# Kernel optimization log

Hardware: AMD Instinct MI355X
Metric: run time of the kernel (lower is better)

The kernel has to match this reference:

```python
import jax, jax.numpy as jnp
import numpy as np

LN_EPS = 1e-12


def _layernorm(x, gamma, beta):
    mu = jnp.mean(x, axis=-1, keepdims=True)
    var = jnp.mean((x - mu) ** 2, axis=-1, keepdims=True)
    return (x - mu) * jax.lax.rsqrt(var + LN_EPS) * gamma + beta


def _gcn(x, node_emb, time_emb, wpool, bpool, ln_g, ln_b):
    # x: [B,N,C]; node_emb: [N,D]; time_emb: [D]
    e = _layernorm(node_emb + time_emb[None, :], ln_g, ln_b)          # [N,D] (dropout in eval = identity)
    adj = jax.nn.softmax(e @ e.T, axis=1)                             # [N,N] dynamic adjacency
    weights = jnp.einsum('nd,dkio->nkio', e, wpool)                   # [N,2,Cin,Cout] per-node weights
    bias = e @ bpool                                                  # [N,Cout]
    # supports = [I, adj]: identity support is just x itself
    x_g = jnp.stack([x, jnp.einsum('nm,bmc->bnc', adj, x)], axis=2)   # [B,N,2,Cin]
    return jnp.einsum('bnki,nkio->bno', x_g, weights) + bias          # [B,N,Cout]


def setup_inputs() -> dict:
    key = jax.random.key(0)
    ks = jax.random.split(key, 10)
    B, N, Cin, H, D = 32, 2048, 32, 64, 64
    s = 0.1
    return {
        'x': jax.random.normal(ks[0], (B, N, Cin), jnp.float32),
        'state': jax.random.normal(ks[1], (B, N, H), jnp.float32),
        'node_embeddings': jax.random.normal(ks[2], (N, D), jnp.float32),
        'time_embeddings': jax.random.normal(ks[3], (D,), jnp.float32),
        'gate_wpool': jax.random.normal(ks[4], (D, 2, Cin + H, 2 * H), jnp.float32) * s,
        'gate_bpool': jax.random.normal(ks[5], (D, 2 * H), jnp.float32) * s,
        'gate_ln_g': jnp.ones((D,), jnp.float32),
        'gate_ln_b': jnp.zeros((D,), jnp.float32),
        'update_wpool': jax.random.normal(ks[6], (D, 2, Cin + H, H), jnp.float32) * s,
        'update_bpool': jax.random.normal(ks[7], (D, H), jnp.float32) * s,
        'update_ln_g': jnp.ones((D,), jnp.float32),
        'update_ln_b': jnp.zeros((D,), jnp.float32),
    }


def reference(x, state, node_embeddings, time_embeddings,
              gate_wpool, gate_bpool, gate_ln_g, gate_ln_b,
              update_wpool, update_bpool, update_ln_g, update_ln_b):
    H = state.shape[-1]
    inp = jnp.concatenate([x, state], axis=-1)                        # [B,N,Cin+H]
    z_r = jax.nn.sigmoid(_gcn(inp, node_embeddings, time_embeddings,
                              gate_wpool, gate_bpool, gate_ln_g, gate_ln_b))
    z, r = z_r[..., :H], z_r[..., H:]
    cand = jnp.concatenate([x, z * state], axis=-1)
    hc = jnp.tanh(_gcn(cand, node_embeddings, time_embeddings,
                       update_wpool, update_bpool, update_ln_g, update_ln_b))
    return r * state + (1.0 - r) * hc
```

## Files before the change

### kernel.cpp

```cpp
#include <hip/hip_runtime.h>

typedef _Float16 f16;
typedef _Float16 half8 __attribute__((ext_vector_type(8)));
typedef float f32x4 __attribute__((ext_vector_type(4)));

#define NN 2048
#define BB 32
#define CINC 32
#define HH 64
#define DD 64
#define C1 96
#define KI 192
#define OG 128
#define OU 64
#define WCG 24576
#define WCU 12288

#define XGI(n, ks, b, kk) (((((size_t)(n)) * 6 + (ks)) * BB + (b)) * 32 + (kk))

__device__ __forceinline__ f32x4 mfma16(half8 a, half8 b, f32x4 c) {
  return __builtin_amdgcn_mfma_f32_16x16x32_f16(a, b, c, 0, 0, 0);
}

typedef __attribute__((address_space(1))) const void* gas_t;
typedef __attribute__((address_space(3))) void* las_t;
__device__ __forceinline__ void gl_lds16(const void* g, void* l) {
  __builtin_amdgcn_global_load_lds((gas_t)g, (las_t)l, 16, 0, 0);
}

#define SWZ(row, kb) (((row) << 7) + ((kb) ^ (((row) & 7) << 4)))

__global__ __launch_bounds__(256) void k_ln_bias(
    const float* __restrict__ ne, const float* __restrict__ te,
    const float* __restrict__ gg, const float* __restrict__ gb,
    const float* __restrict__ ug, const float* __restrict__ ub,
    const float* __restrict__ gbp, const float* __restrict__ ubp,
    float* __restrict__ eg, float* __restrict__ eu,
    f16* __restrict__ egh, f16* __restrict__ euh,
    float* __restrict__ biasg, float* __restrict__ biasu) {
  __shared__ float esg[4][64];
  __shared__ float esu[4][64];
  int nl = threadIdx.x >> 6;
  int node = blockIdx.x * 4 + nl;
  int d = threadIdx.x & 63;
  float v = ne[node * DD + d] + te[d];
  float s = v;
  #pragma unroll
  for (int m = 1; m < 64; m <<= 1) s += __shfl_xor(s, m, 64);
  float mu = s * (1.f / 64.f);
  float df = v - mu;
  float q = df * df;
  #pragma unroll
  for (int m = 1; m < 64; m <<= 1) q += __shfl_xor(q, m, 64);
  float rs = rsqrtf(q * (1.f / 64.f) + 1e-12f);
  float base = df * rs;
  float a = base * gg[d] + gb[d];
  float b = base * ug[d] + ub[d];
  eg[node * DD + d] = a; egh[node * DD + d] = (f16)a;
  eu[node * DD + d] = b; euh[node * DD + d] = (f16)b;
  esg[nl][d] = a; esu[nl][d] = b;
  __syncthreads();
  #pragma unroll
  for (int i = 0; i < 3; ++i) {
    int u = i * 256 + threadIdx.x;
    int un = u / 192, oo = u % 192;
    int n2 = blockIdx.x * 4 + un;
    float acc = 0.f;
    if (oo < OG) {
      #pragma unroll 8
      for (int dd = 0; dd < 64; ++dd) acc += esg[un][dd] * gbp[dd * OG + oo];
      biasg[(size_t)n2 * OG + oo] = acc;
    } else {
      int o = oo - OG;
      #pragma unroll 8
      for (int dd = 0; dd < 64; ++dd) acc += esu[un][dd] * ubp[dd * OU + o];
      biasu[(size_t)n2 * OU + o] = acc;
    }
  }
}

__global__ __launch_bounds__(256) void k_wpool_t(const float* __restrict__ gwp,
                                                 const float* __restrict__ uwp,
                                                 f16* __restrict__ wtg,
                                                 f16* __restrict__ wtu) {
  const int upd = blockIdx.z;
  if (upd && blockIdx.y >= OU / 16) return;
  const float* wpool = upd ? uwp : gwp;
  f16* wt = upd ? wtu : wtg;
  const int O = upd ? OU : OG;
  __shared__ float tile[64][17];
  int ki = blockIdx.x;
  int o0 = blockIdx.y * 16;
  int t = threadIdx.x;
  const int ks = ki >> 5, kk = ki & 31;
  #pragma unroll
  for (int i = 0; i < 4; ++i) {
    int e2 = i * 256 + t;
    int d = e2 >> 4, o = e2 & 15;
    tile[d][o] = wpool[((size_t)d * KI + ki) * O + o0 + o];
  }
  __syncthreads();
  #pragma unroll
  for (int i = 0; i < 4; ++i) {
    int e2 = i * 256 + t;
    int o = e2 >> 6, d = e2 & 63;
    size_t row = ((size_t)ks * O + (o0 + o)) * 32 + kk;
    wt[row * DD + d] = (f16)tile[d][o];
  }
}

__global__ __launch_bounds__(256) void k_build_inp(const float* __restrict__ x,
                                                   const float* __restrict__ st,
                                                   f16* __restrict__ cm,
                                                   f16* __restrict__ xg,
                                                   f16* __restrict__ sth) {
  __shared__ f16 tile[96][66];
  int mb = blockIdx.x * 64;
  int b = blockIdx.y;
  int t = threadIdx.x;
  #pragma unroll
  for (int i = 0; i < 24; ++i) {
    int e2 = i * 256 + t;
    int m = e2 / 96, c = e2 % 96;
    float v = (c < CINC) ? x[((size_t)b * NN + mb + m) * CINC + c]
                         : st[((size_t)b * NN + mb + m) * HH + c - CINC];
    f16 h = (f16)v;
    tile[c][m] = h;
    xg[XGI(mb + m, c >> 5, b, c & 31)] = h;
    if (c >= CINC) sth[((size_t)b * NN + mb + m) * HH + c - CINC] = h;
  }
  __syncthreads();
  #pragma unroll
  for (int i = 0; i < 24; ++i) {
    int e2 = i * 256 + t;
    int c = e2 >> 6, m = e2 & 63;
    cm[((size_t)b * C1 + c) * NN + mb + m] = tile[c][m];
  }
}

__global__ __launch_bounds__(256) void k_transpose_zs(const f16* __restrict__ zs,
                                                      f16* __restrict__ cm) {
  __shared__ f16 tile[64][66];
  int mb = blockIdx.x * 64;
  int b = blockIdx.y;
  int t = threadIdx.x;
  #pragma unroll
  for (int i = 0; i < 16; ++i) {
    int e2 = i * 256 + t;
    int m = e2 >> 6, o = e2 & 63;
    tile[o][m] = zs[((size_t)b * NN + mb + m) * HH + o];
  }
  __syncthreads();
  #pragma unroll
  for (int i = 0; i < 16; ++i) {
    int e2 = i * 256 + t;
    int o = e2 >> 6, m = e2 & 63;
    cm[((size_t)b * C1 + CINC + o) * NN + mb + m] = tile[o][m];
  }
}

__global__ __launch_bounds__(256) void k_scores(const float* __restrict__ e,
                                                float* __restrict__ S) {
  __shared__ float er[32][65];
  __shared__ float ec[32][65];
  int rb = blockIdx.y * 32, cbb = blockIdx.x * 32;
  int t = threadIdx.x;
  {
    int row = t >> 3;
    int d0 = (t & 7) * 8;
    const float* pr = &e[(size_t)(rb + row) * DD + d0];
    const float* pc = &e[(size_t)(cbb + row) * DD + d0];
    #pragma unroll
    for (int j = 0; j < 8; ++j) { er[row][d0 + j] = pr[j]; ec[row][d0 + j] = pc[j]; }
  }
  __syncthreads();
  int r = t >> 5;
  int c = t & 31;
  float a0 = 0.f, a1 = 0.f, a2 = 0.f, a3 = 0.f;
  #pragma unroll 8
  for (int d = 0; d < 64; ++d) {
    float vc = ec[c][d];
    a0 += er[r][d] * vc;
    a1 += er[r + 8][d] * vc;
    a2 += er[r + 16][d] * vc;
    a3 += er[r + 24][d] * vc;
  }
  S[(size_t)(rb + r) * NN + cbb + c] = a0;
  S[(size_t)(rb + r + 8) * NN + cbb + c] = a1;
  S[(size_t)(rb + r + 16) * NN + cbb + c] = a2;
  S[(size_t)(rb + r + 24) * NN + cbb + c] = a3;
}

__global__ __launch_bounds__(256) void k_softmax(const float* __restrict__ S,
                                                 f16* __restrict__ adj) {
  int n = blockIdx.x;
  int t = threadIdx.x;
  const float* row = S + (size_t)n * NN;
  float v[8];
  float mx = -3.0e38f;
  #pragma unroll
  for (int i = 0; i < 8; ++i) { v[i] = row[t + i * 256]; mx = fmaxf(mx, v[i]); }
  #pragma unroll
  for (int m = 1; m < 64; m <<= 1) mx = fmaxf(mx, __shfl_xor(mx, m, 64));
  __shared__ float redm[4];
  if ((t & 63) == 0) redm[t >> 6] = mx;
  __syncthreads();
  mx = fmaxf(fmaxf(redm[0], redm[1]), fmaxf(redm[2], redm[3]));
  float s = 0.f;
  #pragma unroll
  for (int i = 0; i < 8; ++i) { v[i] = expf(v[i] - mx); s += v[i]; }
  #pragma unroll
  for (int m = 1; m < 64; m <<= 1) s += __shfl_xor(s, m, 64);
  __shared__ float reds[4];
  if ((t & 63) == 0) reds[t >> 6] = s;
  __syncthreads();
  s = reds[0] + reds[1] + reds[2] + reds[3];
  float inv = 1.f / s;
  #pragma unroll
  for (int i = 0; i < 8; ++i) adj[(size_t)n * NN + t + i * 256] = (f16)(v[i] * inv);
}

#define BM 64
#define BN 96

__global__ __launch_bounds__(256, 4) void k_gemm_xa(const f16* __restrict__ A,
                                                    const f16* __restrict__ Bm,
                                                    f16* __restrict__ xg) {
  const int orig = blockIdx.x;
  const int xcd = orig & 7, j = orig >> 3;
  const int nb = (j >> 2) * BM;
  const int by = (xcd << 2) + (j & 3);
  const int cb = by * BN;
  const int tid = threadIdx.x;
  const int w = tid >> 6, lane = tid & 63;
  const int wr = (w >> 1) * 32, wc = (w & 1) * 48;
  const int fr = lane & 15, fq = lane >> 4;

  const int arow = tid >> 3;
  const int acolb = ((tid & 7) * 16) ^ ((arow & 7) << 4);
  const char* asrc = (const char*)A + (size_t)(nb + arow) * (NN * 2) + acolb;
  const char* bsrc = (const char*)Bm + (size_t)(cb + arow) * (NN * 2) + acolb;

  __shared__ f16 Al[2][BM * 64];
  __shared__ f16 Bl[2][BN * 64];
  auto stage = [&](int buf, int kt) {
    const size_t ko = (size_t)kt * 2;
    char* ad = (char*)&Al[buf][0] + (w << 10);
    char* bd = (char*)&Bl[buf][0] + (w << 10);
    gl_lds16(asrc + ko, ad);
    gl_lds16(asrc + ko + (size_t)32 * (NN * 2), ad + 4096);
    gl_lds16(bsrc + ko, bd);
    gl_lds16(bsrc + ko + (size_t)32 * (NN * 2), bd + 4096);
    gl_lds16(bsrc + ko + (size_t)64 * (NN * 2), bd + 8192);
  };

  f32x4 acc[2][3] = {};
  stage(0, 0);
  for (int kt = 0; kt < NN; kt += 64) {
    const int cur = (kt >> 6) & 1;
    if (kt + 64 < NN) {
      stage(cur ^ 1, kt + 64);
      asm volatile("s_waitcnt vmcnt(5)" ::: "memory");
    } else {
      asm volatile("s_waitcnt vmcnt(0)" ::: "memory");
    }
    __builtin_amdgcn_sched_barrier(0);
    __builtin_amdgcn_s_barrier();
    const char* Ab = (const char*)&Al[cur][0];
    const char* Bb = (const char*)&Bl[cur][0];
    half8 af[2][2], bf[2][3];
    #pragma unroll
    for (int k0 = 0; k0 < 2; ++k0) {
      const int kb = k0 * 64 + fq * 16;
      #pragma unroll
      for (int mt = 0; mt < 2; ++mt)
        af[k0][mt] = *(const half8*)(Ab + SWZ(wr + mt * 16 + fr, kb));
      #pragma unroll
      for (int nt = 0; nt < 3; ++nt)
        bf[k0][nt] = *(const half8*)(Bb + SWZ(wc + nt * 16 + fr, kb));
    }
    asm volatile("s_waitcnt lgkmcnt(0)" ::: "memory");
    __builtin_amdgcn_sched_barrier(0);
    __builtin_amdgcn_s_barrier();
    #pragma unroll
    for (int k0 = 0; k0 < 2; ++k0)
      #pragma unroll
      for (int mt = 0; mt < 2; ++mt)
        #pragma unroll
        for (int nt = 0; nt < 3; ++nt)
          acc[mt][nt] = mfma16(af[k0][mt], bf[k0][nt], acc[mt][nt]);
  }
  #pragma unroll
  for (int mt = 0; mt < 2; ++mt)
    #pragma unroll
    for (int nt = 0; nt < 3; ++nt)
      #pragma unroll
      for (int r = 0; r < 4; ++r) {
        int n = nb + wr + mt * 16 + fq * 4 + r;
        int l = wc + nt * 16 + fr;
        xg[XGI(n, 3 + (l >> 5), by, l & 31)] = (f16)acc[mt][nt][r];
      }
}

__global__ __launch_bounds__(256) void k_gemm_w2(const f16* __restrict__ A,
                                                 const f16* __restrict__ B,
                                                 f16* __restrict__ W, int ncols) {
  __shared__ f16 Al[128 * 64];
  __shared__ f16 Bl[128 * 64];
  const int cb = blockIdx.x * 128;
  const int nb = blockIdx.y * 128;
  const int tid = threadIdx.x;
  const int w = tid >> 6, lane = tid & 63;
  const int wr = (w >> 1) * 64, wc = (w & 1) * 64;
  const int fr = lane & 15, fq = lane >> 4;
  const int arow = tid >> 3;
  const int acolb = ((tid & 7) * 16) ^ ((arow & 7) << 4);
  const char* asrc = (const char*)A + (size_t)(nb + arow) * 128 + acolb;
  const char* bsrc = (const char*)B + (size_t)(cb + arow) * 128 + acolb;
  char* ad = (char*)Al + (w << 10);
  char* bd = (char*)Bl + (w << 10);
  #pragma unroll
  for (int j = 0; j < 4; ++j) gl_lds16(asrc + (size_t)j * 32 * 128, ad + j * 4096);
  #pragma unroll
  for (int j = 0; j < 4; ++j) gl_lds16(bsrc + (size_t)j * 32 * 128, bd + j * 4096);
  __syncthreads();
  f32x4 acc[4][4] = {};
  #pragma unroll
  for (int k0 = 0; k0 < 2; ++k0) {
    const int kb = k0 * 64 + fq * 16;
    half8 af[4], bf[4];
    #pragma unroll
    for (int mt = 0; mt < 4; ++mt)
      af[mt] = *(const half8*)((const char*)Al + SWZ(wr + mt * 16 + fr, kb));
    #pragma unroll
    for (int nt = 0; nt < 4; ++nt)
      bf[nt] = *(const half8*)((const char*)Bl + SWZ(wc + nt * 16 + fr, kb));
    #pragma unroll
    for (int mt = 0; mt < 4; ++mt)
      #pragma unroll
      for (int nt = 0; nt < 4; ++nt)
        acc[mt][nt] = mfma16(af[mt], bf[nt], acc[mt][nt]);
  }
  #pragma unroll
  for (int mt = 0; mt < 4; ++mt)
    #pragma unroll
    for (int nt = 0; nt < 4; ++nt)
      #pragma unroll
      for (int r = 0; r < 4; ++r) {
        int n = nb + wr + mt * 16 + fq * 4 + r;
        int c = cb + wc + nt * 16 + fr;
        W[(size_t)n * ncols + c] = (f16)acc[mt][nt][r];
      }
}

template <bool GATE>
__global__ __launch_bounds__(256) void k_apply3(
    const f16* __restrict__ xg, const f16* __restrict__ W,
    const float* __restrict__ bias,
    const f16* __restrict__ sth,
    f16* xgw, f16* __restrict__ zs, f16* __restrict__ rbuf,
    float* __restrict__ outp) {
  constexpr int O = GATE ? OG : OU;
  constexpr int WS = GATE ? WCG : WCU;
  constexpr int NOT_ = GATE ? 2 : 1;
  const int n = blockIdx.x;
  const int lane = threadIdx.x & 63, w = threadIdx.x >> 6;
  const int fr = lane & 15, fq = lane >> 4;
  half8 af[2][6];
  #pragma unroll
  for (int mt = 0; mt < 2; ++mt) {
    #pragma unroll
    for (int ks = 0; ks < 6; ++ks)
      af[mt][ks] = *(const half8*)&xg[XGI(n, ks, mt * 16 + fr, fq * 8)];
  }
  if (GATE) __syncthreads();
  f32x4 acc[2][NOT_] = {};
  #pragma unroll
  for (int ks = 0; ks < 6; ++ks) {
    #pragma unroll
    for (int ot = 0; ot < NOT_; ++ot) {
      int o = (GATE ? (w * 2 + ot) : w) * 16 + fr;
      half8 bf = *(const half8*)&W[(size_t)n * WS + (((size_t)ks * O + o) << 5) + fq * 8];
      #pragma unroll
      for (int mt = 0; mt < 2; ++mt) acc[mt][ot] = mfma16(af[mt][ks], bf, acc[mt][ot]);
    }
  }
  #pragma unroll
  for (int mt = 0; mt < 2; ++mt)
    #pragma unroll
    for (int ot = 0; ot < NOT_; ++ot) {
      const int o = (GATE ? (w * 2 + ot) : w) * 16 + fr;
      const float bs = bias[(size_t)n * O + o];
      #pragma unroll
      for (int r = 0; r < 4; ++r) {
        int b = mt * 16 + fq * 4 + r;
        float val = acc[mt][ot][r] + bs;
        if (GATE) {
          float s = 1.f / (1.f + expf(-val));
          if (o < HH) {
            size_t bno = ((size_t)b * NN + n) * HH + o;
            float zst = s * (float)sth[bno];
            xgw[XGI(n, 1 + (o >> 5), b, o & 31)] = (f16)zst;
            zs[bno] = (f16)zst;
          } else {
            rbuf[((size_t)b * NN + n) * HH + (o - HH)] = (f16)s;
          }
        } else {
          size_t bno = ((size_t)b * NN + n) * HH + o;
          float hc = tanhf(val);
          float rr = (float)rbuf[bno];
          outp[bno] = rr * (float)sth[bno] + (1.f - rr) * hc;
        }
      }
    }
}

extern "C" void kernel_launch(void* const* d_in, const int* in_sizes, int n_in,
                              void* d_out, int out_size, void* d_ws, size_t ws_size,
                              hipStream_t stream) {
  const float* x   = (const float*)d_in[0];
  const float* st  = (const float*)d_in[1];
  const float* ne  = (const float*)d_in[2];
  const float* te  = (const float*)d_in[3];
  const float* gwp = (const float*)d_in[4];
  const float* gbp = (const float*)d_in[5];
  const float* gg  = (const float*)d_in[6];
  const float* gb  = (const float*)d_in[7];
  const float* uwp = (const float*)d_in[8];
  const float* ubp = (const float*)d_in[9];
  const float* ug  = (const float*)d_in[10];
  const float* ub  = (const float*)d_in[11];
  float* out = (float*)d_out;

  char* wsb = (char*)d_ws;
  size_t off = 0;
  auto alloc = [&](size_t bytes) {
    char* p = wsb + off;
    off = (off + bytes + 255) & ~(size_t)255;
    return p;
  };
  float* e_g   = (float*)alloc((size_t)NN * DD * 4);
  float* e_u   = (float*)alloc((size_t)NN * DD * 4);
  f16*   egh   = (f16*)  alloc((size_t)NN * DD * 2);
  f16*   euh   = (f16*)  alloc((size_t)NN * DD * 2);
  float* biasg = (float*)alloc((size_t)NN * OG * 4);
  float* biasu = (float*)alloc((size_t)NN * OU * 4);
  f16*   wtg   = (f16*)  alloc((size_t)WCG * DD * 2);
  f16*   wtu   = (f16*)  alloc((size_t)WCU * DD * 2);
  f16*   xg    = (f16*)  alloc((size_t)NN * BB * KI * 2);
  f16*   cm    = (f16*)  alloc((size_t)BB * C1 * NN * 2);
  f16*   zs    = (f16*)  alloc((size_t)BB * NN * HH * 2);
  f16*   rbuf  = (f16*)  alloc((size_t)BB * NN * HH * 2);
  f16*   sth   = (f16*)  alloc((size_t)BB * NN * HH * 2);
  f16*   adj   = (f16*)  alloc((size_t)NN * NN * 2);
  char*  Wreg  =         alloc((size_t)NN * WCG * 2);
  float* S     = (float*)Wreg;
  f16*   W     = (f16*)Wreg;
  (void)ws_size; (void)in_sizes; (void)n_in; (void)out_size;

  hipLaunchKernelGGL(k_ln_bias, dim3(NN / 4), dim3(256), 0, stream,
                     ne, te, gg, gb, ug, ub, gbp, ubp,
                     e_g, e_u, egh, euh, biasg, biasu);
  hipLaunchKernelGGL(k_wpool_t, dim3(KI, OG / 16, 2), dim3(256), 0, stream,
                     gwp, uwp, wtg, wtu);
  hipLaunchKernelGGL(k_build_inp, dim3(NN / 64, BB), dim3(256), 0, stream,
                     x, st, cm, xg, sth);

  hipLaunchKernelGGL(k_scores, dim3(NN / 32, NN / 32), dim3(256), 0, stream, e_g, S);
  hipLaunchKernelGGL(k_softmax, dim3(NN), dim3(256), 0, stream, S, adj);
  hipLaunchKernelGGL(k_gemm_xa, dim3(1024), dim3(256), 0, stream, adj, cm, xg);
  hipLaunchKernelGGL(k_gemm_w2, dim3(WCG / 128, NN / 128), dim3(256), 0, stream,
                     egh, wtg, W, WCG);
  hipLaunchKernelGGL((k_apply3<true>), dim3(NN), dim3(256), 0, stream,
                     xg, W, biasg, sth, xg, zs, rbuf, (float*)nullptr);
  hipLaunchKernelGGL(k_transpose_zs, dim3(NN / 64, BB), dim3(256), 0, stream, zs, cm);

  hipLaunchKernelGGL(k_scores, dim3(NN / 32, NN / 32), dim3(256), 0, stream, e_u, S);
  hipLaunchKernelGGL(k_softmax, dim3(NN), dim3(256), 0, stream, S, adj);
  hipLaunchKernelGGL(k_gemm_xa, dim3(1024), dim3(256), 0, stream, adj, cm, xg);
  hipLaunchKernelGGL(k_gemm_w2, dim3(WCU / 128, NN / 128), dim3(256), 0, stream,
                     euh, wtu, W, WCU);
  hipLaunchKernelGGL((k_apply3<false>), dim3(NN), dim3(256), 0, stream,
                     xg, W, biasu, sth, (f16*)nullptr, (f16*)nullptr, rbuf, out);
}
```

Before: 234.7 us.

## Fuse per-node weight generation into apply kernel, dropping materialized W buffer

Replaces the separate GEMM that materializes per-node weights W (NN x 24576 fp16, ~100MB for gate) plus the apply kernel with a fused kernel. It computes 16 nodes' weight slices into LDS via MFMA and immediately applies them to the batch inputs. Each block handles one 32-wide output quarter for 16 nodes, with blocks mapped by XCD index to share the weight pool. This removes the large global write and read of W. The cost is recomputing weights per output quarter, extra LDS traffic, and two-blocks-per-CU occupancy limits. The z*state write into xg moves into the transpose kernel, and S gets its own buffer.

```diff
diff --git a/kernel.cpp b/kernel.cpp
--- a/kernel.cpp
+++ b/kernel.cpp
@@ -2,6 +2,7 @@
 
 typedef _Float16 f16;
 typedef _Float16 half8 __attribute__((ext_vector_type(8)));
+typedef _Float16 half4 __attribute__((ext_vector_type(4)));
 typedef float f32x4 __attribute__((ext_vector_type(4)));
 
 #define NN 2048
@@ -13,8 +14,6 @@
 #define KI 192
 #define OG 128
 #define OU 64
-#define WCG 24576
-#define WCU 12288
 
 #define XGI(n, ks, b, kk) (((((size_t)(n)) * 6 + (ks)) * BB + (b)) * 32 + (kk))
 
@@ -92,7 +91,6 @@
   int ki = blockIdx.x;
   int o0 = blockIdx.y * 16;
   int t = threadIdx.x;
-  const int ks = ki >> 5, kk = ki & 31;
   #pragma unroll
   for (int i = 0; i < 4; ++i) {
     int e2 = i * 256 + t;
@@ -104,8 +102,7 @@
   for (int i = 0; i < 4; ++i) {
     int e2 = i * 256 + t;
     int o = e2 >> 6, d = e2 & 63;
-    size_t row = ((size_t)ks * O + (o0 + o)) * 32 + kk;
-    wt[row * DD + d] = (f16)tile[d][o];
+    wt[((size_t)(o0 + o) * KI + ki) * DD + d] = (f16)tile[d][o];
   }
 }
 
@@ -139,7 +136,8 @@
 }
 
 __global__ __launch_bounds__(256) void k_transpose_zs(const f16* __restrict__ zs,
-                                                      f16* __restrict__ cm) {
+                                                      f16* __restrict__ cm,
+                                                      f16* __restrict__ xg) {
   __shared__ f16 tile[64][66];
   int mb = blockIdx.x * 64;
   int b = blockIdx.y;
@@ -148,7 +146,9 @@
   for (int i = 0; i < 16; ++i) {
     int e2 = i * 256 + t;
     int m = e2 >> 6, o = e2 & 63;
-    tile[o][m] = zs[((size_t)b * NN + mb + m) * HH + o];
+    f16 v = zs[((size_t)b * NN + mb + m) * HH + o];
+    tile[o][m] = v;
+    xg[XGI(mb + m, 1 + (o >> 5), b, o & 31)] = v;
   }
   __syncthreads();
   #pragma unroll
@@ -302,117 +302,105 @@
       }
 }
 
-__global__ __launch_bounds__(256) void k_gemm_w2(const f16* __restrict__ A,
-                                                 const f16* __restrict__ B,
-                                                 f16* __restrict__ W, int ncols) {
-  __shared__ f16 Al[128 * 64];
-  __shared__ f16 Bl[128 * 64];
-  const int cb = blockIdx.x * 128;
-  const int nb = blockIdx.y * 128;
-  const int tid = threadIdx.x;
-  const int w = tid >> 6, lane = tid & 63;
-  const int wr = (w >> 1) * 64, wc = (w & 1) * 64;
-  const int fr = lane & 15, fq = lane >> 4;
-  const int arow = tid >> 3;
-  const int acolb = ((tid & 7) * 16) ^ ((arow & 7) << 4);
-  const char* asrc = (const char*)A + (size_t)(nb + arow) * 128 + acolb;
-  const char* bsrc = (const char*)B + (size_t)(cb + arow) * 128 + acolb;
-  char* ad = (char*)Al + (w << 10);
-  char* bd = (char*)Bl + (w << 10);
-  #pragma unroll
-  for (int j = 0; j < 4; ++j) gl_lds16(asrc + (size_t)j * 32 * 128, ad + j * 4096);
-  #pragma unroll
-  for (int j = 0; j < 4; ++j) gl_lds16(bsrc + (size_t)j * 32 * 128, bd + j * 4096);
-  __syncthreads();
-  f32x4 acc[4][4] = {};
-  #pragma unroll
-  for (int k0 = 0; k0 < 2; ++k0) {
-    const int kb = k0 * 64 + fq * 16;
-    half8 af[4], bf[4];
-    #pragma unroll
-    for (int mt = 0; mt < 4; ++mt)
-      af[mt] = *(const half8*)((const char*)Al + SWZ(wr + mt * 16 + fr, kb));
-    #pragma unroll
-    for (int nt = 0; nt < 4; ++nt)
-      bf[nt] = *(const half8*)((const char*)Bl + SWZ(wc + nt * 16 + fr, kb));
-    #pragma unroll
-    for (int mt = 0; mt < 4; ++mt)
-      #pragma unroll
-      for (int nt = 0; nt < 4; ++nt)
-        acc[mt][nt] = mfma16(af[mt], bf[nt], acc[mt][nt]);
-  }
-  #pragma unroll
-  for (int mt = 0; mt < 4; ++mt)
-    #pragma unroll
-    for (int nt = 0; nt < 4; ++nt)
-      #pragma unroll
-      for (int r = 0; r < 4; ++r) {
-        int n = nb + wr + mt * 16 + fq * 4 + r;
-        int c = cb + wc + nt * 16 + fr;
-        W[(size_t)n * ncols + c] = (f16)acc[mt][nt][r];
-      }
-}
-
 template <bool GATE>
-__global__ __launch_bounds__(256) void k_apply3(
-    const f16* __restrict__ xg, const f16* __restrict__ W,
+__global__ __launch_bounds__(256, 2) void k_wapply(
+    const f16* __restrict__ eh,
+    const f16* __restrict__ wt,
+    const f16* __restrict__ xg,
     const float* __restrict__ bias,
     const f16* __restrict__ sth,
-    f16* xgw, f16* __restrict__ zs, f16* __restrict__ rbuf,
+    f16* __restrict__ zs, f16* __restrict__ rbuf,
     float* __restrict__ outp) {
   constexpr int O = GATE ? OG : OU;
-  constexpr int WS = GATE ? WCG : WCU;
-  constexpr int NOT_ = GATE ? 2 : 1;
-  const int n = blockIdx.x;
-  const int lane = threadIdx.x & 63, w = threadIdx.x >> 6;
+  __shared__ f16 Wc[16 * 2048];
+  const int id = blockIdx.x;
+  const int xcd = id & 7;
+  int q, nodeblk;
+  if (GATE) { q = xcd >> 1; nodeblk = (id >> 3) * 2 + (xcd & 1); }
+  else      { q = xcd >> 2; nodeblk = (id >> 3) * 4 + (xcd & 3); }
+  const int w = threadIdx.x >> 6, lane = threadIdx.x & 63;
   const int fr = lane & 15, fq = lane >> 4;
-  half8 af[2][6];
-  #pragma unroll
-  for (int mt = 0; mt < 2; ++mt) {
-    #pragma unroll
-    for (int ks = 0; ks < 6; ++ks)
-      af[mt][ks] = *(const half8*)&xg[XGI(n, ks, mt * 16 + fr, fq * 8)];
-  }
-  if (GATE) __syncthreads();
-  f32x4 acc[2][NOT_] = {};
-  #pragma unroll
-  for (int ks = 0; ks < 6; ++ks) {
-    #pragma unroll
-    for (int ot = 0; ot < NOT_; ++ot) {
-      int o = (GATE ? (w * 2 + ot) : w) * 16 + fr;
-      half8 bf = *(const half8*)&W[(size_t)n * WS + (((size_t)ks * O + o) << 5) + fq * 8];
-      #pragma unroll
-      for (int mt = 0; mt < 2; ++mt) acc[mt][ot] = mfma16(af[mt][ks], bf, acc[mt][ot]);
-    }
-  }
-  #pragma unroll
-  for (int mt = 0; mt < 2; ++mt)
-    #pragma unroll
-    for (int ot = 0; ot < NOT_; ++ot) {
-      const int o = (GATE ? (w * 2 + ot) : w) * 16 + fr;
-      const float bs = bias[(size_t)n * O + o];
-      #pragma unroll
-      for (int r = 0; r < 4; ++r) {
-        int b = mt * 16 + fq * 4 + r;
-        float val = acc[mt][ot][r] + bs;
-        if (GATE) {
-          float s = 1.f / (1.f + expf(-val));
-          if (o < HH) {
-            size_t bno = ((size_t)b * NN + n) * HH + o;
-            float zst = s * (float)sth[bno];
-            xgw[XGI(n, 1 + (o >> 5), b, o & 31)] = (f16)zst;
-            zs[bno] = (f16)zst;
-          } else {
-            rbuf[((size_t)b * NN + n) * HH + (o - HH)] = (f16)s;
-          }
-        } else {
-          size_t bno = ((size_t)b * NN + n) * HH + o;
-          float hc = tanhf(val);
-          float rr = (float)rbuf[bno];
-          outp[bno] = rr * (float)sth[bno] + (1.f - rr) * hc;
+  const int nodebase = nodeblk * 16;
+
+  half8 ebf[2];
+  ebf[0] = *(const half8*)&eh[(size_t)(nodebase + fr) * DD + fq * 8];
+  ebf[1] = *(const half8*)&eh[(size_t)(nodebase + fr) * DD + 32 + fq * 8];
+
+  f32x4 acc[4][2][2] = {};
+  for (int c = 0; c < 3; ++c) {
+    #pragma unroll 4
+    for (int tt = 0; tt < 32; ++tt) {
+      const int t = w * 32 + tt;
+      const int o_local = t >> 2;
+      const int kib = (t & 3) * 16;
+      const size_t row = (size_t)(q * 32 + o_local) * KI + c * 64 + kib + fr;
+      const f16* ap = wt + row * DD;
+      half8 a0 = *(const half8*)&ap[fq * 8];
+      half8 a1 = *(const half8*)&ap[32 + fq * 8];
+      f32x4 d = mfma16(a0, ebf[0], f32x4{0.f, 0.f, 0.f, 0.f});
+      d = mfma16(a1, ebf[1], d);
+      half4 h;
+      #pragma unroll
+      for (int r = 0; r < 4; ++r) h[r] = (f16)d[r];
+      const int kil = kib + fq * 4;
+      int byte = fr * 4096 + o_local * 128 + kil * 2;
+      byte ^= (((fr & 7) ^ (o_local & 7)) << 4);
+      *(half4*)((char*)Wc + byte) = h;
+    }
+    __syncthreads();
+    #pragma unroll
+    for (int j = 0; j < 4; ++j) {
+      const int node = w * 4 + j;
+      const int n = nodebase + node;
+      #pragma unroll
+      for (int kb = 0; kb < 2; ++kb) {
+        half8 af[2];
+        #pragma unroll
+        for (int mt = 0; mt < 2; ++mt)
+          af[mt] = *(const half8*)&xg[XGI(n, c * 2 + kb, mt * 16 + fr, fq * 8)];
+        #pragma unroll
+        for (int ot = 0; ot < 2; ++ot) {
+          int byte = node * 4096 + (ot * 16 + fr) * 128 + (kb * 32 + fq * 8) * 2;
+          byte ^= (((node & 7) ^ (fr & 7)) << 4);
+          half8 bf = *(const half8*)((const char*)Wc + byte);
+          #pragma unroll
+          for (int mt = 0; mt < 2; ++mt)
+            acc[j][mt][ot] = mfma16(af[mt], bf, acc[j][mt][ot]);
         }
       }
     }
+    __syncthreads();
+  }
+  #pragma unroll
+  for (int j = 0; j < 4; ++j) {
+    const int n = nodebase + w * 4 + j;
+    #pragma unroll
+    for (int ot = 0; ot < 2; ++ot) {
+      const int og = q * 32 + ot * 16 + fr;
+      const float bs = bias[(size_t)n * O + og];
+      #pragma unroll
+      for (int mt = 0; mt < 2; ++mt)
+        #pragma unroll
+        for (int r = 0; r < 4; ++r) {
+          const int b = mt * 16 + fq * 4 + r;
+          const float val = acc[j][mt][ot][r] + bs;
+          if (GATE) {
+            const float s = 1.f / (1.f + expf(-val));
+            if (q < 2) {
+              const size_t bno = ((size_t)b * NN + n) * HH + og;
+              zs[bno] = (f16)(s * (float)sth[bno]);
+            } else {
+              rbuf[((size_t)b * NN + n) * HH + (og - HH)] = (f16)s;
+            }
+          } else {
+            const size_t bno = ((size_t)b * NN + n) * HH + og;
+            const float hc = tanhf(val);
+            const float rr = (float)rbuf[bno];
+            outp[bno] = rr * (float)sth[bno] + (1.f - rr) * hc;
+          }
+        }
+    }
+  }
 }
 
 extern "C" void kernel_launch(void* const* d_in, const int* in_sizes, int n_in,
@@ -445,17 +433,15 @@
   f16*   euh   = (f16*)  alloc((size_t)NN * DD * 2);
   float* biasg = (float*)alloc((size_t)NN * OG * 4);
   float* biasu = (float*)alloc((size_t)NN * OU * 4);
-  f16*   wtg   = (f16*)  alloc((size_t)WCG * DD * 2);
-  f16*   wtu   = (f16*)  alloc((size_t)WCU * DD * 2);
+  f16*   wtg   = (f16*)  alloc((size_t)OG * KI * DD * 2);
+  f16*   wtu   = (f16*)  alloc((size_t)OU * KI * DD * 2);
   f16*   xg    = (f16*)  alloc((size_t)NN * BB * KI * 2);
   f16*   cm    = (f16*)  alloc((size_t)BB * C1 * NN * 2);
   f16*   zs    = (f16*)  alloc((size_t)BB * NN * HH * 2);
   f16*   rbuf  = (f16*)  alloc((size_t)BB * NN * HH * 2);
   f16*   sth   = (f16*)  alloc((size_t)BB * NN * HH * 2);
   f16*   adj   = (f16*)  alloc((size_t)NN * NN * 2);
-  char*  Wreg  =         alloc((size_t)NN * WCG * 2);
-  float* S     = (float*)Wreg;
-  f16*   W     = (f16*)Wreg;
+  float* S     = (float*)alloc((size_t)NN * NN * 4);
   (void)ws_size; (void)in_sizes; (void)n_in; (void)out_size;
 
   hipLaunchKernelGGL(k_ln_bias, dim3(NN / 4), dim3(256), 0, stream,
@@ -469,17 +455,14 @@
   hipLaunchKernelGGL(k_scores, dim3(NN / 32, NN / 32), dim3(256), 0, stream, e_g, S);
   hipLaunchKernelGGL(k_softmax, dim3(NN), dim3(256), 0, stream, S, adj);
   hipLaunchKernelGGL(k_gemm_xa, dim3(1024), dim3(256), 0, stream, adj, cm, xg);
-  hipLaunchKernelGGL(k_gemm_w2, dim3(WCG / 128, NN / 128), dim3(256), 0, stream,
-                     egh, wtg, W, WCG);
-  hipLaunchKernelGGL((k_apply3<true>), dim3(NN), dim3(256), 0, stream,
-                     xg, W, biasg, sth, xg, zs, rbuf, (float*)nullptr);
-  hipLaunchKernelGGL(k_transpose_zs, dim3(NN / 64, BB), dim3(256), 0, stream, zs, cm);
+  hipLaunchKernelGGL((k_wapply<true>), dim3(512), dim3(256), 0, stream,
+                     egh, wtg, xg, biasg, sth, zs, rbuf, (float*)nullptr);
+  hipLaunchKernelGGL(k_transpose_zs, dim3(NN / 64, BB), dim3(256), 0, stream,
+                     zs, cm, xg);
 
   hipLaunchKernelGGL(k_scores, dim3(NN / 32, NN / 32), dim3(256), 0, stream, e_u, S);
   hipLaunchKernelGGL(k_softmax, dim3(NN), dim3(256), 0, stream, S, adj);
   hipLaunchKernelGGL(k_gemm_xa, dim3(1024), dim3(256), 0, stream, adj, cm, xg);
-  hipLaunchKernelGGL(k_gemm_w2, dim3(WCU / 128, NN / 128), dim3(256), 0, stream,
-                     euh, wtu, W, WCU);
-  hipLaunchKernelGGL((k_apply3<false>), dim3(NN), dim3(256), 0, stream,
-                     xg, W, biasu, sth, (f16*)nullptr, (f16*)nullptr, rbuf, out);
-}
+  hipLaunchKernelGGL((k_wapply<false>), dim3(256), dim3(256), 0, stream,
+                     euh, wtu, xg, biasu, sth, (f16*)nullptr, rbuf, out);
+}
```

Result: slower. 311.5 us (+32.7%).

## Fuse score matmul and softmax into one MFMA online-softmax kernel

Applied to the files above, without the earlier changes.

Replaces the fp32 scalar score kernel and the separate row-softmax kernel with a single kernel that computes e·eᵀ in fp16 MFMA tiles. It keeps a running max and sum per row, then recomputes the scores to write normalized fp16 adjacency. This removes the 16 MB fp32 score matrix round trip through memory and the fp32 embedding copies, at the cost of doing the dot products twice, computing scores from fp16 embeddings, and using the fast __expf. The per-node apply kernel also loads all weight fragments up front before issuing MFMAs, to overlap those loads.

```diff
diff --git a/kernel.cpp b/kernel.cpp
--- a/kernel.cpp
+++ b/kernel.cpp
@@ -35,7 +35,6 @@
     const float* __restrict__ gg, const float* __restrict__ gb,
     const float* __restrict__ ug, const float* __restrict__ ub,
     const float* __restrict__ gbp, const float* __restrict__ ubp,
-    float* __restrict__ eg, float* __restrict__ eu,
     f16* __restrict__ egh, f16* __restrict__ euh,
     float* __restrict__ biasg, float* __restrict__ biasu) {
   __shared__ float esg[4][64];
@@ -56,8 +55,8 @@
   float base = df * rs;
   float a = base * gg[d] + gb[d];
   float b = base * ug[d] + ub[d];
-  eg[node * DD + d] = a; egh[node * DD + d] = (f16)a;
-  eu[node * DD + d] = b; euh[node * DD + d] = (f16)b;
+  egh[node * DD + d] = (f16)a;
+  euh[node * DD + d] = (f16)b;
   esg[nl][d] = a; esu[nl][d] = b;
   __syncthreads();
   #pragma unroll
@@ -159,65 +158,70 @@
   }
 }
 
-__global__ __launch_bounds__(256) void k_scores(const float* __restrict__ e,
-                                                float* __restrict__ S) {
-  __shared__ float er[32][65];
-  __shared__ float ec[32][65];
-  int rb = blockIdx.y * 32, cbb = blockIdx.x * 32;
-  int t = threadIdx.x;
-  {
-    int row = t >> 3;
-    int d0 = (t & 7) * 8;
-    const float* pr = &e[(size_t)(rb + row) * DD + d0];
-    const float* pc = &e[(size_t)(cbb + row) * DD + d0];
-    #pragma unroll
-    for (int j = 0; j < 8; ++j) { er[row][d0 + j] = pr[j]; ec[row][d0 + j] = pc[j]; }
-  }
-  __syncthreads();
-  int r = t >> 5;
-  int c = t & 31;
-  float a0 = 0.f, a1 = 0.f, a2 = 0.f, a3 = 0.f;
-  #pragma unroll 8
-  for (int d = 0; d < 64; ++d) {
-    float vc = ec[c][d];
-    a0 += er[r][d] * vc;
-    a1 += er[r + 8][d] * vc;
-    a2 += er[r + 16][d] * vc;
-    a3 += er[r + 24][d] * vc;
-  }
-  S[(size_t)(rb + r) * NN + cbb + c] = a0;
-  S[(size_t)(rb + r + 8) * NN + cbb + c] = a1;
-  S[(size_t)(rb + r + 16) * NN + cbb + c] = a2;
-  S[(size_t)(rb + r + 24) * NN + cbb + c] = a3;
-}
-
-__global__ __launch_bounds__(256) void k_softmax(const float* __restrict__ S,
-                                                 f16* __restrict__ adj) {
-  int n = blockIdx.x;
-  int t = threadIdx.x;
-  const float* row = S + (size_t)n * NN;
-  float v[8];
-  float mx = -3.0e38f;
-  #pragma unroll
-  for (int i = 0; i < 8; ++i) { v[i] = row[t + i * 256]; mx = fmaxf(mx, v[i]); }
-  #pragma unroll
-  for (int m = 1; m < 64; m <<= 1) mx = fmaxf(mx, __shfl_xor(mx, m, 64));
-  __shared__ float redm[4];
-  if ((t & 63) == 0) redm[t >> 6] = mx;
-  __syncthreads();
-  mx = fmaxf(fmaxf(redm[0], redm[1]), fmaxf(redm[2], redm[3]));
-  float s = 0.f;
-  #pragma unroll
-  for (int i = 0; i < 8; ++i) { v[i] = expf(v[i] - mx); s += v[i]; }
-  #pragma unroll
-  for (int m = 1; m < 64; m <<= 1) s += __shfl_xor(s, m, 64);
-  __shared__ float reds[4];
-  if ((t & 63) == 0) reds[t >> 6] = s;
-  __syncthreads();
-  s = reds[0] + reds[1] + reds[2] + reds[3];
-  float inv = 1.f / s;
-  #pragma unroll
-  for (int i = 0; i < 8; ++i) adj[(size_t)n * NN + t + i * 256] = (f16)(v[i] * inv);
+__global__ __launch_bounds__(256) void k_attn(const f16* __restrict__ eh,
+                                              f16* __restrict__ adj) {
+  const int r0 = blockIdx.x * 16;
+  const int w = threadIdx.x >> 6, lane = threadIdx.x & 63;
+  const int fr = lane & 15, fq = lane >> 4;
+  __shared__ float pm[4][16], ps[4][16];
+  __shared__ float fm[16], fs[16];
+  const half8 a0 = *(const half8*)&eh[(size_t)(r0 + fr) * DD + fq * 8];
+  const half8 a1 = *(const half8*)&eh[(size_t)(r0 + fr) * DD + 32 + fq * 8];
+  float m[4], s[4];
+  #pragma unroll
+  for (int r = 0; r < 4; ++r) { m[r] = -3.0e38f; s[r] = 0.f; }
+  for (int ct = 0; ct < 32; ++ct) {
+    const int c0 = w * 512 + ct * 16;
+    half8 b0 = *(const half8*)&eh[(size_t)(c0 + fr) * DD + fq * 8];
+    half8 b1 = *(const half8*)&eh[(size_t)(c0 + fr) * DD + 32 + fq * 8];
+    f32x4 d = mfma16(a0, b0, f32x4{0.f, 0.f, 0.f, 0.f});
+    d = mfma16(a1, b1, d);
+    #pragma unroll
+    for (int r = 0; r < 4; ++r) {
+      float mn = fmaxf(m[r], d[r]);
+      s[r] = s[r] * __expf(m[r] - mn) + __expf(d[r] - mn);
+      m[r] = mn;
+    }
+  }
+  #pragma unroll
+  for (int r = 0; r < 4; ++r) {
+    #pragma unroll
+    for (int mk = 1; mk < 16; mk <<= 1) {
+      float mo = __shfl_xor(m[r], mk, 64);
+      float so = __shfl_xor(s[r], mk, 64);
+      float mn = fmaxf(m[r], mo);
+      s[r] = s[r] * __expf(m[r] - mn) + so * __expf(mo - mn);
+      m[r] = mn;
+    }
+  }
+  if (fr == 0) {
+    #pragma unroll
+    for (int r = 0; r < 4; ++r) { pm[w][fq * 4 + r] = m[r]; ps[w][fq * 4 + r] = s[r]; }
+  }
+  __syncthreads();
+  if (threadIdx.x < 16) {
+    float M = -3.0e38f;
+    #pragma unroll
+    for (int i = 0; i < 4; ++i) M = fmaxf(M, pm[i][threadIdx.x]);
+    float S = 0.f;
+    #pragma unroll
+    for (int i = 0; i < 4; ++i) S += ps[i][threadIdx.x] * __expf(pm[i][threadIdx.x] - M);
+    fm[threadIdx.x] = M; fs[threadIdx.x] = 1.f / S;
+  }
+  __syncthreads();
+  float Mr[4], Sr[4];
+  #pragma unroll
+  for (int r = 0; r < 4; ++r) { Mr[r] = fm[fq * 4 + r]; Sr[r] = fs[fq * 4 + r]; }
+  for (int ct = 0; ct < 32; ++ct) {
+    const int c0 = w * 512 + ct * 16;
+    half8 b0 = *(const half8*)&eh[(size_t)(c0 + fr) * DD + fq * 8];
+    half8 b1 = *(const half8*)&eh[(size_t)(c0 + fr) * DD + 32 + fq * 8];
+    f32x4 d = mfma16(a0, b0, f32x4{0.f, 0.f, 0.f, 0.f});
+    d = mfma16(a1, b1, d);
+    #pragma unroll
+    for (int r = 0; r < 4; ++r)
+      adj[(size_t)(r0 + fq * 4 + r) * NN + c0 + fr] = (f16)(__expf(d[r] - Mr[r]) * Sr[r]);
+  }
 }
 
 #define BM 64
@@ -374,17 +378,23 @@
       af[mt][ks] = *(const half8*)&xg[XGI(n, ks, mt * 16 + fr, fq * 8)];
   }
   if (GATE) __syncthreads();
-  f32x4 acc[2][NOT_] = {};
+  half8 bf[6][NOT_];
   #pragma unroll
   for (int ks = 0; ks < 6; ++ks) {
     #pragma unroll
     for (int ot = 0; ot < NOT_; ++ot) {
       int o = (GATE ? (w * 2 + ot) : w) * 16 + fr;
-      half8 bf = *(const half8*)&W[(size_t)n * WS + (((size_t)ks * O + o) << 5) + fq * 8];
-      #pragma unroll
-      for (int mt = 0; mt < 2; ++mt) acc[mt][ot] = mfma16(af[mt][ks], bf, acc[mt][ot]);
-    }
-  }
+      bf[ks][ot] = *(const half8*)&W[(size_t)n * WS + (((size_t)ks * O + o) << 5) + fq * 8];
+    }
+  }
+  f32x4 acc[2][NOT_] = {};
+  #pragma unroll
+  for (int ks = 0; ks < 6; ++ks)
+    #pragma unroll
+    for (int ot = 0; ot < NOT_; ++ot)
+      #pragma unroll
+      for (int mt = 0; mt < 2; ++mt)
+        acc[mt][ot] = mfma16(af[mt][ks], bf[ks][ot], acc[mt][ot]);
   #pragma unroll
   for (int mt = 0; mt < 2; ++mt)
     #pragma unroll
@@ -439,8 +449,6 @@
     off = (off + bytes + 255) & ~(size_t)255;
     return p;
   };
-  float* e_g   = (float*)alloc((size_t)NN * DD * 4);
-  float* e_u   = (float*)alloc((size_t)NN * DD * 4);
   f16*   egh   = (f16*)  alloc((size_t)NN * DD * 2);
   f16*   euh   = (f16*)  alloc((size_t)NN * DD * 2);
   float* biasg = (float*)alloc((size_t)NN * OG * 4);
@@ -453,21 +461,18 @@
   f16*   rbuf  = (f16*)  alloc((size_t)BB * NN * HH * 2);
   f16*   sth   = (f16*)  alloc((size_t)BB * NN * HH * 2);
   f16*   adj   = (f16*)  alloc((size_t)NN * NN * 2);
-  char*  Wreg  =         alloc((size_t)NN * WCG * 2);
-  float* S     = (float*)Wreg;
-  f16*   W     = (f16*)Wreg;
+  f16*   W     = (f16*)  alloc((size_t)NN * WCG * 2);
   (void)ws_size; (void)in_sizes; (void)n_in; (void)out_size;
 
   hipLaunchKernelGGL(k_ln_bias, dim3(NN / 4), dim3(256), 0, stream,
                      ne, te, gg, gb, ug, ub, gbp, ubp,
-                     e_g, e_u, egh, euh, biasg, biasu);
+                     egh, euh, biasg, biasu);
   hipLaunchKernelGGL(k_wpool_t, dim3(KI, OG / 16, 2), dim3(256), 0, stream,
                      gwp, uwp, wtg, wtu);
   hipLaunchKernelGGL(k_build_inp, dim3(NN / 64, BB), dim3(256), 0, stream,
                      x, st, cm, xg, sth);
 
-  hipLaunchKernelGGL(k_scores, dim3(NN / 32, NN / 32), dim3(256), 0, stream, e_g, S);
-  hipLaunchKernelGGL(k_softmax, dim3(NN), dim3(256), 0, stream, S, adj);
+  hipLaunchKernelGGL(k_attn, dim3(NN / 16), dim3(256), 0, stream, egh, adj);
   hipLaunchKernelGGL(k_gemm_xa, dim3(1024), dim3(256), 0, stream, adj, cm, xg);
   hipLaunchKernelGGL(k_gemm_w2, dim3(WCG / 128, NN / 128), dim3(256), 0, stream,
                      egh, wtg, W, WCG);
@@ -475,8 +480,7 @@
                      xg, W, biasg, sth, xg, zs, rbuf, (float*)nullptr);
   hipLaunchKernelGGL(k_transpose_zs, dim3(NN / 64, BB), dim3(256), 0, stream, zs, cm);
 
-  hipLaunchKernelGGL(k_scores, dim3(NN / 32, NN / 32), dim3(256), 0, stream, e_u, S);
-  hipLaunchKernelGGL(k_softmax, dim3(NN), dim3(256), 0, stream, S, adj);
+  hipLaunchKernelGGL(k_attn, dim3(NN / 16), dim3(256), 0, stream, euh, adj);
   hipLaunchKernelGGL(k_gemm_xa, dim3(1024), dim3(256), 0, stream, adj, cm, xg);
   hipLaunchKernelGGL(k_gemm_w2, dim3(WCU / 128, NN / 128), dim3(256), 0, stream,
                      euh, wtu, W, WCU);
```

Result: faster. 222.5 us (-5.2%).
